# Kernel optimization log

Measured on AMD Instinct MI355X. Metric: run time of the kernel, lower is better.

## Reference

```python
import jax, jax.numpy as jnp
import numpy as np

N, E, H = 25000, 100000, 32          # nodes, edges, node/clique hidden dim
NC, A, EC = 8000, 50000, 24000       # cliques, node2clique assignments, clique edges
EEMB, CEE, L = 8, 8, 2               # edge emb dims, n layers


def segment_mean(vals, ids, num):
    s = jax.ops.segment_sum(vals, ids, num_segments=num)
    cnt = jax.ops.segment_sum(jnp.ones(ids.shape[0], vals.dtype), ids, num_segments=num)
    return s / jnp.maximum(cnt, 1.0)[:, None]


def setup_inputs() -> dict:
    key = jax.random.key(0)
    ks = jax.random.split(key, 24)
    s = 0.1  # param scale
    inp = {
        "node_features": jax.random.normal(ks[0], (N, H), jnp.float32),
        "edge_index": jax.random.randint(ks[1], (2, E), 0, N),
        "edge_features": jax.random.normal(ks[2], (E, EEMB), jnp.float32),
        "clique_features": jax.random.normal(ks[3], (NC, H), jnp.float32),
        "node2clique_index": jnp.stack([
            jax.random.randint(ks[4], (A,), 0, N),
            jax.random.randint(ks[5], (A,), 0, NC)]),
        "clique_edge_index": jax.random.randint(ks[6], (2, EC), 0, NC),
        "clique_edge_features": jax.random.normal(ks[7], (EC, CEE), jnp.float32),
        # node NNConv params (stacked over L layers)
        "nn1_w": jax.random.normal(ks[8], (L, EEMB, H)) * s,
        "nn1_b": jnp.zeros((L, H)),
        "nn2_w": jax.random.normal(ks[9], (L, H, H * H)) * s,
        "nn2_b": jnp.zeros((L, H * H)),
        "root_w": jax.random.normal(ks[10], (L, H, H)) * s,
        "root_b": jnp.zeros((L, H)),
        # Node2Clique linear
        "n2c_w": jax.random.normal(ks[11], (L, H, H)) * s,
        "n2c_b": jnp.zeros((L, H)),
        # clique NNConv params
        "cnn1_w": jax.random.normal(ks[12], (L, CEE, H)) * s,
        "cnn1_b": jnp.zeros((L, H)),
        "cnn2_w": jax.random.normal(ks[13], (L, H, H * H)) * s,
        "cnn2_b": jnp.zeros((L, H * H)),
        "croot_w": jax.random.normal(ks[14], (L, H, H)) * s,
        "croot_b": jnp.zeros((L, H)),
        # Clique2Node linear
        "c2n_w": jax.random.normal(ks[15], (L, H, H)) * s,
        "c2n_b": jnp.zeros((L, H)),
    }
    return inp


def nnconv(x, src, dst, edge_attr, w1, b1, w2, b2, rw, rb, n_out_nodes):
    # per-edge weight matrices from the edge MLP: [E, in, out]
    h = jax.nn.relu(edge_attr @ w1 + b1)
    We = (h @ w2 + b2).reshape(edge_attr.shape[0], x.shape[1], -1)
    msg = jnp.einsum('ei,eio->eo', x[src], We)           # message from source
    agg = segment_mean(msg, dst, n_out_nodes)            # mean aggregation at target
    return agg + x @ rw + rb                             # root weight + bias


def reference(node_features, edge_index, edge_features, clique_features,
              node2clique_index, clique_edge_index, clique_edge_features,
              nn1_w, nn1_b, nn2_w, nn2_b, root_w, root_b, n2c_w, n2c_b,
              cnn1_w, cnn1_b, cnn2_w, cnn2_b, croot_w, croot_b, c2n_w, c2n_b):
    x, c = node_features, clique_features
    src, dst = edge_index[0], edge_index[1]
    nid, cid = node2clique_index[0], node2clique_index[1]
    csrc, cdst = clique_edge_index[0], clique_edge_index[1]
    for l in range(L):
        # node-level edge-conditioned conv
        x = jax.nn.relu(nnconv(x, src, dst, edge_features,
                               nn1_w[l], nn1_b[l], nn2_w[l], nn2_b[l],
                               root_w[l], root_b[l], N))
        # Node2Clique: project node feats, scatter-mean into cliques
        m = x @ n2c_w[l] + n2c_b[l]
        c = c + segment_mean(m[nid], cid, NC)
        # clique-level edge-conditioned conv
        c = jax.nn.relu(nnconv(c, csrc, cdst, clique_edge_features,
                               cnn1_w[l], cnn1_b[l], cnn2_w[l], cnn2_b[l],
                               croot_w[l], croot_b[l], NC))
        # Clique2Node: project clique feats, scatter-mean back onto nodes
        m = c @ c2n_w[l] + c2n_b[l]
        x = x + segment_mean(m[cid], nid, N)
    return (x, c)
```

## Files before the change

### kernel.cpp

```cpp
#include <hip/hip_runtime.h>
#include <hip/hip_bf16.h>

typedef unsigned int u32;
typedef unsigned short u16;

#define DEVINL __device__ __forceinline__

constexpr int Nn  = 25000;
constexpr int Ee  = 100000;
constexpr int NCc = 8000;
constexpr int Aa  = 50000;
constexpr int ECc = 24000;
constexpr int TCOLS = 1088;
constexpr int WPSZ  = TCOLS*32;
constexpr int NSTR  = 580;
constexpr int NB_N = (Nn + 255)/256;
constexpr int NB_C = (NCc + 255)/256;

typedef float f32x4 __attribute__((ext_vector_type(4)));
typedef short s16x8 __attribute__((ext_vector_type(8)));

DEVINL float b2f(u16 u){ union{u32 i;float f;}v; v.i = ((u32)u)<<16; return v.f; }
DEVINL float bfl(u32 u){ union{u32 i;float f;}v; v.i = u<<16; return v.f; }
DEVINL float bfh(u32 u){ union{u32 i;float f;}v; v.i = u & 0xffff0000u; return v.f; }
DEVINL u16 f2b(float f){ union{float f;u32 i;}v; v.f=f; u32 i=v.i;
  return (u16)((i + 0x7fffu + ((i>>16)&1u)) >> 16); }
DEVINL u32 pk2(float a, float b){ return (u32)f2b(a) | ((u32)f2b(b) << 16); }
DEVINL float ldw(const void* p, long i, int f){
  return f ? ((const float*)p)[i] : b2f(((const u16*)p)[i]);
}

__global__ __launch_bounds__(256) void k_detect(const u16* __restrict__ p, int n,
                        u32* __restrict__ maxbits, int* __restrict__ zcnt,
                        int* __restrict__ done, int* __restrict__ flag){
  int i0 = blockIdx.x*256 + threadIdx.x;
  float lm = 0.f; int lz = 0;
  for (int i = i0; i < n; i += gridDim.x*256){
    u16 v = p[i];
    if (v == 0) lz++;
    lm = fmaxf(lm, fabsf(b2f(v)));
  }
  #pragma unroll
  for (int off = 32; off; off >>= 1){
    lm = fmaxf(lm, __shfl_down(lm, off));
    lz += __shfl_down(lz, off);
  }
  if ((threadIdx.x & 63) == 0){
    atomicMax(maxbits, __float_as_uint(lm));
    atomicAdd(zcnt, lz);
  }
  __syncthreads();
  if (threadIdx.x == 0){
    __threadfence();
    if (atomicAdd(done, 1) == gridDim.x - 1){
      float m = __uint_as_float(*maxbits);
      *flag = (m > 1e6f || *zcnt > n/4) ? 1 : 0;
    }
  }
}

__global__ __launch_bounds__(256) void k_conv_all(const void* __restrict__ xin, const void* __restrict__ cin,
                         float* __restrict__ xA, float* __restrict__ cA, const int* __restrict__ flag){
  int i = blockIdx.x*256 + threadIdx.x;
  int f = *flag;
  if (i < Nn*32) xA[i] = ldw(xin, i, f);
  else { i -= Nn*32; if (i < NCc*32) cA[i] = ldw(cin, i, f); }
}

__global__ __launch_bounds__(256) void k_count_all(const int* __restrict__ ei, const int* __restrict__ cei,
                          const int* __restrict__ n2c,
                          int* __restrict__ deg_nd, int* __restrict__ deg_ce,
                          int* __restrict__ deg_n2c, int* __restrict__ deg_c2n,
                          int* __restrict__ cnt_sn, int* __restrict__ cnt_sc){
  int i = blockIdx.x*256 + threadIdx.x;
  if (i < Ee)                             atomicAdd(&deg_nd[ei[Ee + i]], 1);
  else if ((i -= Ee) < ECc)               atomicAdd(&deg_ce[cei[ECc + i]], 1);
  else if ((i -= ECc) < Aa)               atomicAdd(&deg_n2c[n2c[Aa + i]], 1);
  else if ((i -= Aa) < Aa)                atomicAdd(&deg_c2n[n2c[i]], 1);
  else if ((i -= Aa) < Ee)                atomicAdd(&cnt_sn[ei[i]], 1);
  else if ((i -= Ee) < ECc)               atomicAdd(&cnt_sc[cei[i]], 1);
}

__global__ __launch_bounds__(256) void k_scan_block(
    const int* __restrict__ c0, const int* __restrict__ c1,
    const int* __restrict__ c2, const int* __restrict__ c3,
    int* __restrict__ o0, int* __restrict__ o1, int* __restrict__ o2, int* __restrict__ o3,
    int* __restrict__ b0, int* __restrict__ b1, int* __restrict__ b2, int* __restrict__ b3){
  __shared__ int s[256];
  int bid = blockIdx.x, seg, rb;
  if (bid < NB_N){ seg=0; rb=bid; }
  else if (bid < NB_N+NB_C){ seg=1; rb=bid-NB_N; }
  else if (bid < 2*NB_N+NB_C){ seg=2; rb=bid-NB_N-NB_C; }
  else { seg=3; rb=bid-2*NB_N-NB_C; }
  const int* cnt = seg==0?c0 : seg==1?c1 : seg==2?c2 : c3;
  int* offs = seg==0?o0 : seg==1?o1 : seg==2?o2 : o3;
  int* bs   = seg==0?b0 : seg==1?b1 : seg==2?b2 : b3;
  int M = (seg & 1) ? NCc : Nn;
  int tid = threadIdx.x;
  int i = rb*256 + tid;
  int v = (i < M) ? cnt[i] : 0;
  s[tid] = v; __syncthreads();
  for (int d = 1; d < 256; d <<= 1){
    int t = (tid >= d) ? s[tid-d] : 0;
    __syncthreads();
    s[tid] += t;
    __syncthreads();
  }
  if (i < M) offs[i] = s[tid] - v;
  if (tid == 255) bs[rb] = s[255];
}

__global__ __launch_bounds__(512) void k_spine(int* __restrict__ b0, int* __restrict__ b1,
                      int* __restrict__ b2, int* __restrict__ b3){
  __shared__ int s[512];
  int tid = threadIdx.x, seg = tid >> 7, lane = tid & 127;
  int NB = (seg & 1) ? NB_C : NB_N;
  int* bp = seg==0?b0 : seg==1?b1 : seg==2?b2 : b3;
  int v = (lane < NB) ? bp[lane] : 0;
  s[tid] = v; __syncthreads();
  for (int d = 1; d < 128; d <<= 1){
    int t = (lane >= d) ? s[tid-d] : 0;
    __syncthreads();
    s[tid] += t;
    __syncthreads();
  }
  if (lane < NB) bp[lane] = s[tid] - v;
}

__global__ __launch_bounds__(256) void k_scan_fix(
    int* __restrict__ o0, int* __restrict__ o1, int* __restrict__ o2, int* __restrict__ o3,
    const int* __restrict__ b0, const int* __restrict__ b1,
    const int* __restrict__ b2, const int* __restrict__ b3){
  int i = blockIdx.x*256 + threadIdx.x;
  if (i < Nn) o0[i] += b0[i >> 8];
  else if ((i -= Nn) < NCc) o1[i] += b1[i >> 8];
  else if ((i -= NCc) < Nn) o2[i] += b2[i >> 8];
  else if ((i -= Nn) < NCc) o3[i] += b3[i >> 8];
}

__global__ __launch_bounds__(256) void k_place(const int* __restrict__ ei, const int* __restrict__ cei,
                      const int* __restrict__ n2c,
                      const int* __restrict__ offs_n, const int* __restrict__ offs_c,
                      const int* __restrict__ offs_an, const int* __restrict__ offs_ac,
                      int* __restrict__ cur_n, int* __restrict__ cur_c,
                      int* __restrict__ cur_an, int* __restrict__ cur_ac,
                      int* __restrict__ perm_n, int* __restrict__ perm_c,
                      int* __restrict__ an2c, int* __restrict__ ac2n){
  int i = blockIdx.x*256 + threadIdx.x;
  if (i < Ee){
    int s = ei[i];
    perm_n[offs_n[s] + atomicAdd(&cur_n[s], 1)] = i;
  } else if ((i -= Ee) < ECc){
    int s = cei[i];
    perm_c[offs_c[s] + atomicAdd(&cur_c[s], 1)] = i;
  } else if ((i -= ECc) < Aa){
    int c = n2c[Aa + i];
    an2c[offs_ac[c] + atomicAdd(&cur_ac[c], 1)] = n2c[i];
  } else if ((i -= Aa) < Aa){
    int nd = n2c[i];
    ac2n[offs_an[nd] + atomicAdd(&cur_an[nd], 1)] = n2c[Aa + i];
  }
}

__global__ __launch_bounds__(256) void k_gather(const int* __restrict__ ei, const int* __restrict__ cei,
                       const int* __restrict__ perm_n, const int* __restrict__ perm_c,
                       const void* __restrict__ ef, const void* __restrict__ cef,
                       const int* __restrict__ flag,
                       int2* __restrict__ sdp_n, float* __restrict__ efp_n,
                       int2* __restrict__ sdp_c, float* __restrict__ efp_c){
  int i = blockIdx.x*256 + threadIdx.x;
  int f = *flag;
  if (i < Ee*8){
    int p = i >> 3, j = i & 7;
    int e = perm_n[p];
    efp_n[i] = ldw(ef, (long)e*8 + j, f);
    if (j == 0) sdp_n[p] = make_int2(ei[e], ei[Ee + e]);
  } else if ((i -= Ee*8) < ECc*8){
    int p = i >> 3, j = i & 7;
    int e = perm_c[p];
    efp_c[i] = ldw(cef, (long)e*8 + j, f);
    if (j == 0) sdp_c[p] = make_int2(cei[e], cei[ECc + e]);
  }
}

__global__ __launch_bounds__(256) void k_wpack_all(const void* __restrict__ nn2w, const void* __restrict__ nn2b,
                          const void* __restrict__ rootw,
                          const void* __restrict__ cnn2w, const void* __restrict__ cnn2b,
                          const void* __restrict__ crootw,
                          const int* __restrict__ flag, u16* __restrict__ Wp4){
  int i = blockIdx.x*256 + threadIdx.x;
  if (i >= 4*WPSZ) return;
  int set = i / WPSZ, j = i - set*WPSZ;
  int l = set >> 1, isC = set & 1;
  const void* W2 = isC ? cnn2w : nn2w;
  const void* B2 = isC ? cnn2b : nn2b;
  const void* RW = isC ? crootw : rootw;
  int f = *flag;
  int col = j >> 5, ii = j & 31;
  float v;
  if (col < 1024)      v = ldw(W2, (long)l*32768 + ((col>>5)<<10) + (ii<<5) + (col&31), f);
  else if (col < 1056) v = ldw(B2, (long)l*1024 + (ii<<5) + (col-1024), f);
  else                 v = ldw(RW, (long)l*1024 + (ii<<5) + (col-1056), f);
  Wp4[i] = f2b(v);
}

__global__ __launch_bounds__(512) void k_conv_fused(const float* __restrict__ base, int M,
                           const int2* __restrict__ sdp, const float* __restrict__ efp,
                           const int* __restrict__ offs, int E_,
                           const void* __restrict__ w1, long w1off,
                           const void* __restrict__ b1, long b1off,
                           const u16* __restrict__ Wp,
                           const void* __restrict__ rb, long rboff,
                           const int* __restrict__ flag,
                           float* __restrict__ feat_root, float* __restrict__ agg){
  __shared__ __align__(16) u32 Ts[16*NSTR];
  __shared__ float w1s[256];
  __shared__ __align__(8) u32 hws[8][4][16];
  int tid = threadIdx.x;
  int w = tid >> 6, lane = tid & 63;
  int quad = lane >> 4, lm = lane & 15;
  int n0 = blockIdx.x * 16;
  int f = *flag;
  if (tid < 256) w1s[tid] = ldw(w1, w1off + tid, f);
  float bb0 = ldw(b1, b1off + 2*lm, f);
  float bb1 = ldw(b1, b1off + 2*lm + 1, f);
  int n = n0 + lm;
  int nc = n < M ? n : M-1;
  const float* bp = base + (size_t)nc*32 + quad*8;
  s16x8 bfrag;
  #pragma unroll
  for (int j = 0; j < 8; j++) bfrag[j] = (short)f2b(bp[j]);
  #pragma unroll 1
  for (int ti = 0; ti < 9; ti++){
    int ct = w*9 + ti;
    if (ct >= 68) break;
    int colbase = ct*16;
    s16x8 afrag = *(const s16x8*)(Wp + (size_t)(colbase + lm)*32 + quad*8);
    f32x4 acc = {0.f, 0.f, 0.f, 0.f};
    acc = __builtin_amdgcn_mfma_f32_16x16x32_bf16(afrag, bfrag, acc, 0, 0, 0);
    if (ct < 66){
      int k = ct >> 1;
      int p0 = (ct & 1)*8 + quad*2;
      int idx = lm*NSTR + p0*36 + k;
      Ts[idx]      = pk2(acc[0], acc[1]);
      Ts[idx + 36] = pk2(acc[2], acc[3]);
    } else if (n < M){
      int o = (ct - 66)*16 + quad*4 - 0;
      o = (colbase + quad*4) - 1056;
      float4 v = make_float4(acc[0] + ldw(rb, rboff+o,   f),
                             acc[1] + ldw(rb, rboff+o+1, f),
                             acc[2] + ldw(rb, rboff+o+2, f),
                             acc[3] + ldw(rb, rboff+o+3, f));
      *(float4*)&feat_root[(size_t)n*32 + o] = v;
    }
  }
  __syncthreads();
  int lo = offs[n0];
  int hi = (n0 + 16 < M) ? offs[n0 + 16] : E_;
  int eg = quad, kk = lm;
  int pos = lo + w*4;
  float ef0 = 0.f, ef1 = 0.f; int sd0 = 0, sd1 = 0;
  if (lane < 32){
    int idx = pos*8 + lane;        if (idx < hi*8) ef0 = efp[idx];
    idx = (pos+32)*8 + lane;       if (idx < hi*8) ef1 = efp[idx];
  } else if (lane < 40){
    int idx = pos*2 + (lane-32);   if (idx < hi*2) sd0 = ((const int*)sdp)[idx];
    idx = (pos+32)*2 + (lane-32);  if (idx < hi*2) sd1 = ((const int*)sdp)[idx];
  }
  for (; pos < hi; pos += 32){
    int np = pos + 64;
    float ef2 = 0.f; int sd2 = 0;
    if (lane < 32){ int idx = np*8 + lane; if (idx < hi*8) ef2 = efp[idx]; }
    else if (lane < 40){ int idx = np*2 + (lane-32); if (idx < hi*2) sd2 = ((const int*)sdp)[idx]; }
    int sn = __shfl(sd0, 32 + 2*eg);
    int dn = __shfl(sd0, 33 + 2*eg);
    bool valid = (pos + eg < hi);
    int sr = sn - n0; sr = sr < 0 ? 0 : (sr > 15 ? 15 : sr);
    float a0 = bb0, a1 = bb1;
    #pragma unroll
    for (int j = 0; j < 8; j++){
      float ev = __shfl(ef0, eg*8 + j);
      a0 += ev * w1s[j*32 + 2*kk];
      a1 += ev * w1s[j*32 + 2*kk+1];
    }
    hws[w][eg][kk] = pk2(fmaxf(a0, 0.f), fmaxf(a1, 0.f));
    if (valid){
      const u32* Tr = &Ts[sr*NSTR + kk*36];
      u32 vb = Tr[32];
      float m0 = bfl(vb), m1 = bfh(vb);
      #pragma unroll
      for (int g = 0; g < 8; g++){
        uint4 tv = *(const uint4*)&Tr[g*4];
        uint2 hp = *(const uint2*)&hws[w][eg][g*2];
        float h0 = bfl(hp.x), h1 = bfh(hp.x), h2 = bfl(hp.y), h3 = bfh(hp.y);
        m0 += h0*bfl(tv.x) + h1*bfl(tv.y) + h2*bfl(tv.z) + h3*bfl(tv.w);
        m1 += h0*bfh(tv.x) + h1*bfh(tv.y) + h2*bfh(tv.z) + h3*bfh(tv.w);
      }
      float* ap = agg + (size_t)dn*32 + 2*kk;
      atomicAdd(ap,   m0);
      atomicAdd(ap+1, m1);
    }
    ef0 = ef1; sd0 = sd1; ef1 = ef2; sd1 = sd2;
  }
}

__global__ __launch_bounds__(256) void k_update_lin(const float* __restrict__ agg, const int* __restrict__ deg,
                           const float* __restrict__ feat_root, int M,
                           const void* __restrict__ w, long woff,
                           const void* __restrict__ b, long boff,
                           const int* __restrict__ flag,
                           float* __restrict__ feat, void* __restrict__ dt_out, long dt_off,
                           float* __restrict__ m_out){
  __shared__ float wsm[1024], bs[32], rows[8][33];
  int tid = threadIdx.x;
  int f = *flag;
  for (int idx = tid; idx < 1024; idx += 256) wsm[idx] = ldw(w, woff + idx, f);
  if (tid < 32) bs[tid] = ldw(b, boff + tid, f);
  int nl = tid >> 5, o = tid & 31;
  int n = blockIdx.x*8 + nl;
  long i = (long)n*32 + o;
  if (n < M){
    int dg = deg[n];
    float d = (float)(dg > 1 ? dg : 1);
    float v = fmaxf(agg[i]/d + feat_root[i], 0.f);
    rows[nl][o] = v;
    if (feat) feat[i] = v;
    if (dt_out){
      if (f) ((float*)dt_out)[dt_off + i] = v;
      else   ((u16*)dt_out)[dt_off + i]   = f2b(v);
    }
  }
  __syncthreads();
  if (n >= M) return;
  float acc = bs[o];
  #pragma unroll
  for (int j = 0; j < 32; j++) acc += rows[nl][j]*wsm[j*32+o];
  m_out[i] = acc;
}

__global__ __launch_bounds__(256) void k_segmean(const float* __restrict__ base, const float* __restrict__ m,
                        const int* __restrict__ idxarr, const int* __restrict__ offs,
                        const int* __restrict__ deg, int M, float* __restrict__ out){
  int i = blockIdx.x*256 + threadIdx.x;
  if (i >= M*32) return;
  int c = i >> 5, o = i & 31;
  int lo = offs[c], cnt = deg[c];
  float s = 0.f;
  for (int a = lo; a < lo + cnt; a++) s += m[(size_t)idxarr[a]*32 + o];
  out[i] = base[i] + s/(float)(cnt > 1 ? cnt : 1);
}

__global__ __launch_bounds__(256) void k_segmean_out(const float* __restrict__ base, const float* __restrict__ m,
                        const int* __restrict__ idxarr, const int* __restrict__ offs,
                        const int* __restrict__ deg, int M,
                        void* __restrict__ out, const int* __restrict__ flag){
  int i = blockIdx.x*256 + threadIdx.x;
  if (i >= M*32) return;
  int c = i >> 5, o = i & 31;
  int lo = offs[c], cnt = deg[c];
  float s = 0.f;
  for (int a = lo; a < lo + cnt; a++) s += m[(size_t)idxarr[a]*32 + o];
  float v = base[i] + s/(float)(cnt > 1 ? cnt : 1);
  if (*flag) ((float*)out)[i] = v;
  else       ((u16*)out)[i]   = f2b(v);
}

extern "C" void kernel_launch(void* const* d_in, const int* in_sizes, int n_in,
                              void* d_out, int out_size, void* d_ws, size_t ws_size,
                              hipStream_t stream){
  const int* ei  = (const int*)d_in[1];
  const int* n2c = (const int*)d_in[4];
  const int* cei = (const int*)d_in[5];
  const void *efr = d_in[2], *cefr = d_in[6];
  const void *nn1w = d_in[7], *nn1b = d_in[8], *nn2w = d_in[9], *nn2b = d_in[10],
             *rootw = d_in[11], *rootb = d_in[12], *n2cw = d_in[13], *n2cb = d_in[14],
             *cnn1w = d_in[15], *cnn1b = d_in[16], *cnn2w = d_in[17], *cnn2b = d_in[18],
             *crootw = d_in[19], *crootb = d_in[20], *c2nw = d_in[21], *c2nb = d_in[22];

  char* ws = (char*)d_ws;
  size_t off = 0;
  auto alloc = [&](size_t bytes){ void* p = ws + off; off += (bytes + 255) & ~(size_t)255; return p; };

  size_t zstart = off;
  float* aggE0  = (float*)alloc((size_t)Nn*32*4);
  float* aggE1  = (float*)alloc((size_t)Nn*32*4);
  float* caggE0 = (float*)alloc((size_t)NCc*32*4);
  float* caggE1 = (float*)alloc((size_t)NCc*32*4);
  int* deg_nd  = (int*)alloc((size_t)Nn*4);
  int* deg_ce  = (int*)alloc((size_t)NCc*4);
  int* deg_n2c = (int*)alloc((size_t)NCc*4);
  int* deg_c2n = (int*)alloc((size_t)Nn*4);
  int* cnt_sn  = (int*)alloc((size_t)Nn*4);
  int* cnt_sc  = (int*)alloc((size_t)NCc*4);
  int* cur_n   = (int*)alloc((size_t)Nn*4);
  int* cur_c   = (int*)alloc((size_t)NCc*4);
  int* cur_an  = (int*)alloc((size_t)Nn*4);
  int* cur_ac  = (int*)alloc((size_t)NCc*4);
  u32* maxbits = (u32*)alloc(256);
  int* zcnt = (int*)((char*)maxbits + 4);
  int* flag = (int*)((char*)maxbits + 8);
  int* done = (int*)((char*)maxbits + 12);
  size_t zbytes = off - zstart;

  float* xA  = (float*)alloc((size_t)Nn*32*4);
  float* xB  = (float*)alloc((size_t)Nn*32*4);
  float* xA1 = (float*)alloc((size_t)Nn*32*4);
  float* xC  = (float*)alloc((size_t)Nn*32*4);
  float* cA  = (float*)alloc((size_t)NCc*32*4);
  float* cB  = (float*)alloc((size_t)NCc*32*4);
  float* cC0 = (float*)alloc((size_t)NCc*32*4);
  float* cB1 = (float*)alloc((size_t)NCc*32*4);
  float* m_n = (float*)alloc((size_t)Nn*32*4);
  float* m_c = (float*)alloc((size_t)NCc*32*4);
  float* frn = (float*)alloc((size_t)Nn*32*4);
  float* frc = (float*)alloc((size_t)NCc*32*4);
  int* offs_n  = (int*)alloc((size_t)Nn*4);
  int* offs_c  = (int*)alloc((size_t)NCc*4);
  int* offs_an = (int*)alloc((size_t)Nn*4);
  int* offs_ac = (int*)alloc((size_t)NCc*4);
  int* bsum0 = (int*)alloc(512);
  int* bsum1 = (int*)alloc(512);
  int* bsum2 = (int*)alloc(512);
  int* bsum3 = (int*)alloc(512);
  int* perm_n = (int*)alloc((size_t)Ee*4);
  int* perm_c = (int*)alloc((size_t)ECc*4);
  int* an2c = (int*)alloc((size_t)Aa*4);
  int* ac2n = (int*)alloc((size_t)Aa*4);
  int2* sdp_n = (int2*)alloc((size_t)Ee*8);
  int2* sdp_c = (int2*)alloc((size_t)ECc*8);
  float* efp_n = (float*)alloc((size_t)Ee*8*4);
  float* efp_c = (float*)alloc((size_t)ECc*8*4);
  u16* Wp4 = (u16*)alloc((size_t)4*WPSZ*2);

  auto nb = [](int n){ return (n + 255)/256; };

  hipMemsetAsync(ws + zstart, 0, zbytes, stream);
  k_detect<<<256,256,0,stream>>>((const u16*)d_in[0], Nn*32, maxbits, zcnt, done, flag);
  k_conv_all<<<nb(Nn*32 + NCc*32),256,0,stream>>>(d_in[0], d_in[3], xA, cA, flag);
  k_count_all<<<nb(2*Ee + 2*ECc + 2*Aa),256,0,stream>>>(ei, cei, n2c,
      deg_nd, deg_ce, deg_n2c, deg_c2n, cnt_sn, cnt_sc);
  k_scan_block<<<2*(NB_N+NB_C),256,0,stream>>>(cnt_sn, cnt_sc, deg_c2n, deg_n2c,
      offs_n, offs_c, offs_an, offs_ac, bsum0, bsum1, bsum2, bsum3);
  k_spine<<<1,512,0,stream>>>(bsum0, bsum1, bsum2, bsum3);
  k_scan_fix<<<nb(2*(Nn+NCc)),256,0,stream>>>(offs_n, offs_c, offs_an, offs_ac,
      bsum0, bsum1, bsum2, bsum3);
  k_place<<<nb(Ee+ECc+2*Aa),256,0,stream>>>(ei, cei, n2c, offs_n, offs_c, offs_an, offs_ac,
      cur_n, cur_c, cur_an, cur_ac, perm_n, perm_c, an2c, ac2n);
  k_gather<<<nb(8*(Ee+ECc)),256,0,stream>>>(ei, cei, perm_n, perm_c, efr, cefr, flag,
      sdp_n, efp_n, sdp_c, efp_c);
  k_wpack_all<<<nb(4*WPSZ),256,0,stream>>>(nn2w, nn2b, rootw, cnn2w, cnn2b, crootw, flag, Wp4);

  int Gn = (Nn + 15)/16, Gc = (NCc + 15)/16;

  k_conv_fused<<<Gn,512,0,stream>>>(xA, Nn, sdp_n, efp_n, offs_n, Ee,
      nn1w, 0, nn1b, 0, Wp4 + 0*WPSZ, rootb, 0, flag, frn, aggE0);
  k_update_lin<<<(Nn+7)/8,256,0,stream>>>(aggE0, deg_nd, frn, Nn, n2cw, 0, n2cb, 0, flag,
      xB, nullptr, 0, m_n);
  k_segmean<<<nb(NCc*32),256,0,stream>>>(cA, m_n, an2c, offs_ac, deg_n2c, NCc, cB);
  k_conv_fused<<<Gc,512,0,stream>>>(cB, NCc, sdp_c, efp_c, offs_c, ECc,
      cnn1w, 0, cnn1b, 0, Wp4 + 1*WPSZ, crootb, 0, flag, frc, caggE0);
  k_update_lin<<<(NCc+7)/8,256,0,stream>>>(caggE0, deg_ce, frc, NCc, c2nw, 0, c2nb, 0, flag,
      cC0, nullptr, 0, m_c);
  k_segmean<<<nb(Nn*32),256,0,stream>>>(xB, m_c, ac2n, offs_an, deg_c2n, Nn, xA1);
  k_conv_fused<<<Gn,512,0,stream>>>(xA1, Nn, sdp_n, efp_n, offs_n, Ee,
      nn1w, 256, nn1b, 32, Wp4 + 2*WPSZ, rootb, 32, flag, frn, aggE1);
  k_update_lin<<<(Nn+7)/8,256,0,stream>>>(aggE1, deg_nd, frn, Nn, n2cw, 1024, n2cb, 32, flag,
      xC, nullptr, 0, m_n);
  k_segmean<<<nb(NCc*32),256,0,stream>>>(cC0, m_n, an2c, offs_ac, deg_n2c, NCc, cB1);
  k_conv_fused<<<Gc,512,0,stream>>>(cB1, NCc, sdp_c, efp_c, offs_c, ECc,
      cnn1w, 256, cnn1b, 32, Wp4 + 3*WPSZ, crootb, 32, flag, frc, caggE1);
  k_update_lin<<<(NCc+7)/8,256,0,stream>>>(caggE1, deg_ce, frc, NCc, c2nw, 1024, c2nb, 32, flag,
      nullptr, d_out, (long)Nn*32, m_c);
  k_segmean_out<<<nb(Nn*32),256,0,stream>>>(xC, m_c, ac2n, offs_an, deg_c2n, Nn, d_out, flag);
}
```

Measured before the change: 351.1 us.

## Fuse segment-mean scatters into update kernel and fold mean into conv prologue

Removes the separate segment-mean kernels: the update/linear kernel now scatters its projected rows with atomics into per-target accumulators, and the next conv kernel adds the accumulator divided by degree while loading its input. The initial input-conversion kernel is dropped, with conv reading raw inputs directly, and a final store kernel writes both outputs. The shared-memory T layout is changed to a plain bf16 row layout with a simpler single-stage prefetch. The atomic scatters add contention and nondeterministic summation order, and the new accumulator buffers must be zeroed.

```diff
diff --git a/kernel.cpp b/kernel.cpp
--- a/kernel.cpp
+++ b/kernel.cpp
@@ -13,7 +13,7 @@
 constexpr int ECc = 24000;
 constexpr int TCOLS = 1088;
 constexpr int WPSZ  = TCOLS*32;
-constexpr int NSTR  = 580;
+constexpr int TSP   = 1064;
 constexpr int NB_N = (Nn + 255)/256;
 constexpr int NB_C = (NCc + 255)/256;
 
@@ -57,14 +57,6 @@
       *flag = (m > 1e6f || *zcnt > n/4) ? 1 : 0;
     }
   }
-}
-
-__global__ __launch_bounds__(256) void k_conv_all(const void* __restrict__ xin, const void* __restrict__ cin,
-                         float* __restrict__ xA, float* __restrict__ cA, const int* __restrict__ flag){
-  int i = blockIdx.x*256 + threadIdx.x;
-  int f = *flag;
-  if (i < Nn*32) xA[i] = ldw(xin, i, f);
-  else { i -= Nn*32; if (i < NCc*32) cA[i] = ldw(cin, i, f); }
 }
 
 __global__ __launch_bounds__(256) void k_count_all(const int* __restrict__ ei, const int* __restrict__ cei,
@@ -204,7 +196,8 @@
   Wp4[i] = f2b(v);
 }
 
-__global__ __launch_bounds__(512) void k_conv_fused(const float* __restrict__ base, int M,
+__global__ __launch_bounds__(512) void k_conv_fused(const void* __restrict__ base, int braw,
+                           const float* __restrict__ addagg, const int* __restrict__ adddeg, int M,
                            const int2* __restrict__ sdp, const float* __restrict__ efp,
                            const int* __restrict__ offs, int E_,
                            const void* __restrict__ w1, long w1off,
@@ -213,7 +206,7 @@
                            const void* __restrict__ rb, long rboff,
                            const int* __restrict__ flag,
                            float* __restrict__ feat_root, float* __restrict__ agg){
-  __shared__ __align__(16) u32 Ts[16*NSTR];
+  __shared__ __align__(16) u16 Ts[16*TSP];
   __shared__ float w1s[256];
   __shared__ __align__(8) u32 hws[8][4][16];
   int tid = threadIdx.x;
@@ -221,15 +214,26 @@
   int quad = lane >> 4, lm = lane & 15;
   int n0 = blockIdx.x * 16;
   int f = *flag;
+  int bf = braw ? f : 1;
   if (tid < 256) w1s[tid] = ldw(w1, w1off + tid, f);
   float bb0 = ldw(b1, b1off + 2*lm, f);
   float bb1 = ldw(b1, b1off + 2*lm + 1, f);
   int n = n0 + lm;
   int nc = n < M ? n : M-1;
-  const float* bp = base + (size_t)nc*32 + quad*8;
+  long bidx = (long)nc*32 + quad*8;
+  float fv[8];
+  #pragma unroll
+  for (int j = 0; j < 8; j++) fv[j] = ldw(base, bidx + j, bf);
+  if (addagg){
+    int dg = adddeg[nc];
+    float d = (float)(dg > 1 ? dg : 1);
+    const float* ap = addagg + (size_t)nc*32 + quad*8;
+    #pragma unroll
+    for (int j = 0; j < 8; j++) fv[j] += ap[j]/d;
+  }
   s16x8 bfrag;
   #pragma unroll
-  for (int j = 0; j < 8; j++) bfrag[j] = (short)f2b(bp[j]);
+  for (int j = 0; j < 8; j++) bfrag[j] = (short)f2b(fv[j]);
   #pragma unroll 1
   for (int ti = 0; ti < 9; ti++){
     int ct = w*9 + ti;
@@ -238,15 +242,13 @@
     s16x8 afrag = *(const s16x8*)(Wp + (size_t)(colbase + lm)*32 + quad*8);
     f32x4 acc = {0.f, 0.f, 0.f, 0.f};
     acc = __builtin_amdgcn_mfma_f32_16x16x32_bf16(afrag, bfrag, acc, 0, 0, 0);
+    int cb = colbase + quad*4;
     if (ct < 66){
-      int k = ct >> 1;
-      int p0 = (ct & 1)*8 + quad*2;
-      int idx = lm*NSTR + p0*36 + k;
-      Ts[idx]      = pk2(acc[0], acc[1]);
-      Ts[idx + 36] = pk2(acc[2], acc[3]);
+      u32 lo = (u32)f2b(acc[0]) | ((u32)f2b(acc[1]) << 16);
+      u32 hi = (u32)f2b(acc[2]) | ((u32)f2b(acc[3]) << 16);
+      *(uint2*)&Ts[lm*TSP + cb] = make_uint2(lo, hi);
     } else if (n < M){
-      int o = (ct - 66)*16 + quad*4 - 0;
-      o = (colbase + quad*4) - 1056;
+      int o = cb - 1056;
       float4 v = make_float4(acc[0] + ldw(rb, rboff+o,   f),
                              acc[1] + ldw(rb, rboff+o+1, f),
                              acc[2] + ldw(rb, rboff+o+2, f),
@@ -259,48 +261,44 @@
   int hi = (n0 + 16 < M) ? offs[n0 + 16] : E_;
   int eg = quad, kk = lm;
   int pos = lo + w*4;
-  float ef0 = 0.f, ef1 = 0.f; int sd0 = 0, sd1 = 0;
-  if (lane < 32){
-    int idx = pos*8 + lane;        if (idx < hi*8) ef0 = efp[idx];
-    idx = (pos+32)*8 + lane;       if (idx < hi*8) ef1 = efp[idx];
-  } else if (lane < 40){
-    int idx = pos*2 + (lane-32);   if (idx < hi*2) sd0 = ((const int*)sdp)[idx];
-    idx = (pos+32)*2 + (lane-32);  if (idx < hi*2) sd1 = ((const int*)sdp)[idx];
-  }
+  float efv = 0.f; int sdv = 0;
+  if (lane < 32){ int idx = pos*8 + lane; if (idx < hi*8) efv = efp[idx]; }
+  else if (lane < 40){ int idx = pos*2 + (lane-32); if (idx < hi*2) sdv = ((const int*)sdp)[idx]; }
   for (; pos < hi; pos += 32){
-    int np = pos + 64;
-    float ef2 = 0.f; int sd2 = 0;
-    if (lane < 32){ int idx = np*8 + lane; if (idx < hi*8) ef2 = efp[idx]; }
-    else if (lane < 40){ int idx = np*2 + (lane-32); if (idx < hi*2) sd2 = ((const int*)sdp)[idx]; }
-    int sn = __shfl(sd0, 32 + 2*eg);
-    int dn = __shfl(sd0, 33 + 2*eg);
+    int np = pos + 32;
+    float efv_n = 0.f; int sdv_n = 0;
+    if (lane < 32){ int idx = np*8 + lane; if (idx < hi*8) efv_n = efp[idx]; }
+    else if (lane < 40){ int idx = np*2 + (lane-32); if (idx < hi*2) sdv_n = ((const int*)sdp)[idx]; }
+    int sn = __shfl(sdv, 32 + 2*eg);
+    int dn = __shfl(sdv, 33 + 2*eg);
     bool valid = (pos + eg < hi);
     int sr = sn - n0; sr = sr < 0 ? 0 : (sr > 15 ? 15 : sr);
     float a0 = bb0, a1 = bb1;
     #pragma unroll
     for (int j = 0; j < 8; j++){
-      float ev = __shfl(ef0, eg*8 + j);
+      float ev = __shfl(efv, eg*8 + j);
       a0 += ev * w1s[j*32 + 2*kk];
       a1 += ev * w1s[j*32 + 2*kk+1];
     }
     hws[w][eg][kk] = pk2(fmaxf(a0, 0.f), fmaxf(a1, 0.f));
     if (valid){
-      const u32* Tr = &Ts[sr*NSTR + kk*36];
-      u32 vb = Tr[32];
+      const u16* Tr = &Ts[sr*TSP];
+      u32 vb = *(const u32*)&Tr[1024 + 2*kk];
       float m0 = bfl(vb), m1 = bfh(vb);
       #pragma unroll
-      for (int g = 0; g < 8; g++){
-        uint4 tv = *(const uint4*)&Tr[g*4];
-        uint2 hp = *(const uint2*)&hws[w][eg][g*2];
-        float h0 = bfl(hp.x), h1 = bfh(hp.x), h2 = bfl(hp.y), h3 = bfh(hp.y);
-        m0 += h0*bfl(tv.x) + h1*bfl(tv.y) + h2*bfl(tv.z) + h3*bfl(tv.w);
-        m1 += h0*bfh(tv.x) + h1*bfh(tv.y) + h2*bfh(tv.z) + h3*bfh(tv.w);
+      for (int kq = 0; kq < 16; kq++){
+        u32 hp = hws[w][eg][kq];
+        float h0 = bfl(hp), h1 = bfh(hp);
+        u32 v0 = *(const u32*)&Tr[(2*kq)*32 + 2*kk];
+        u32 v1 = *(const u32*)&Tr[(2*kq+1)*32 + 2*kk];
+        m0 += h0*bfl(v0) + h1*bfl(v1);
+        m1 += h0*bfh(v0) + h1*bfh(v1);
       }
       float* ap = agg + (size_t)dn*32 + 2*kk;
       atomicAdd(ap,   m0);
       atomicAdd(ap+1, m1);
     }
-    ef0 = ef1; sd0 = sd1; ef1 = ef2; sd1 = sd2;
+    efv = efv_n; sdv = sdv_n;
   }
 }
 
@@ -309,8 +307,9 @@
                            const void* __restrict__ w, long woff,
                            const void* __restrict__ b, long boff,
                            const int* __restrict__ flag,
-                           float* __restrict__ feat, void* __restrict__ dt_out, long dt_off,
-                           float* __restrict__ m_out){
+                           float* __restrict__ feat,
+                           const int* __restrict__ sidx, const int* __restrict__ soffs,
+                           const int* __restrict__ sdeg, float* __restrict__ sagg){
   __shared__ float wsm[1024], bs[32], rows[8][33];
   int tid = threadIdx.x;
   int f = *flag;
@@ -324,43 +323,31 @@
     float d = (float)(dg > 1 ? dg : 1);
     float v = fmaxf(agg[i]/d + feat_root[i], 0.f);
     rows[nl][o] = v;
-    if (feat) feat[i] = v;
-    if (dt_out){
-      if (f) ((float*)dt_out)[dt_off + i] = v;
-      else   ((u16*)dt_out)[dt_off + i]   = f2b(v);
-    }
+    feat[i] = v;
   }
   __syncthreads();
   if (n >= M) return;
   float acc = bs[o];
   #pragma unroll
   for (int j = 0; j < 32; j++) acc += rows[nl][j]*wsm[j*32+o];
-  m_out[i] = acc;
-}
-
-__global__ __launch_bounds__(256) void k_segmean(const float* __restrict__ base, const float* __restrict__ m,
-                        const int* __restrict__ idxarr, const int* __restrict__ offs,
-                        const int* __restrict__ deg, int M, float* __restrict__ out){
-  int i = blockIdx.x*256 + threadIdx.x;
-  if (i >= M*32) return;
-  int c = i >> 5, o = i & 31;
-  int lo = offs[c], cnt = deg[c];
-  float s = 0.f;
-  for (int a = lo; a < lo + cnt; a++) s += m[(size_t)idxarr[a]*32 + o];
-  out[i] = base[i] + s/(float)(cnt > 1 ? cnt : 1);
-}
-
-__global__ __launch_bounds__(256) void k_segmean_out(const float* __restrict__ base, const float* __restrict__ m,
-                        const int* __restrict__ idxarr, const int* __restrict__ offs,
-                        const int* __restrict__ deg, int M,
-                        void* __restrict__ out, const int* __restrict__ flag){
-  int i = blockIdx.x*256 + threadIdx.x;
-  if (i >= M*32) return;
-  int c = i >> 5, o = i & 31;
-  int lo = offs[c], cnt = deg[c];
-  float s = 0.f;
-  for (int a = lo; a < lo + cnt; a++) s += m[(size_t)idxarr[a]*32 + o];
-  float v = base[i] + s/(float)(cnt > 1 ? cnt : 1);
+  int slo = soffs[n], scnt = sdeg[n];
+  for (int a = 0; a < scnt; a++)
+    atomicAdd(&sagg[(size_t)sidx[slo + a]*32 + o], acc);
+}
+
+__global__ __launch_bounds__(256) void k_store(const float* __restrict__ x, const float* __restrict__ xagg,
+                      const int* __restrict__ xdeg, const float* __restrict__ c,
+                      void* __restrict__ out, const int* __restrict__ flag){
+  int i = blockIdx.x*256 + threadIdx.x;
+  int tot = Nn*32 + NCc*32;
+  if (i >= tot) return;
+  float v;
+  if (i < Nn*32){
+    int n = i >> 5;
+    int dg = xdeg[n];
+    float d = (float)(dg > 1 ? dg : 1);
+    v = x[i] + xagg[i]/d;
+  } else v = c[i - Nn*32];
   if (*flag) ((float*)out)[i] = v;
   else       ((u16*)out)[i]   = f2b(v);
 }
@@ -386,6 +373,10 @@
   float* aggE1  = (float*)alloc((size_t)Nn*32*4);
   float* caggE0 = (float*)alloc((size_t)NCc*32*4);
   float* caggE1 = (float*)alloc((size_t)NCc*32*4);
+  float* caggS0 = (float*)alloc((size_t)NCc*32*4);
+  float* caggS1 = (float*)alloc((size_t)NCc*32*4);
+  float* aggS0  = (float*)alloc((size_t)Nn*32*4);
+  float* aggS1  = (float*)alloc((size_t)Nn*32*4);
   int* deg_nd  = (int*)alloc((size_t)Nn*4);
   int* deg_ce  = (int*)alloc((size_t)NCc*4);
   int* deg_n2c = (int*)alloc((size_t)NCc*4);
@@ -402,26 +393,18 @@
   int* done = (int*)((char*)maxbits + 12);
   size_t zbytes = off - zstart;
 
-  float* xA  = (float*)alloc((size_t)Nn*32*4);
   float* xB  = (float*)alloc((size_t)Nn*32*4);
-  float* xA1 = (float*)alloc((size_t)Nn*32*4);
   float* xC  = (float*)alloc((size_t)Nn*32*4);
-  float* cA  = (float*)alloc((size_t)NCc*32*4);
-  float* cB  = (float*)alloc((size_t)NCc*32*4);
   float* cC0 = (float*)alloc((size_t)NCc*32*4);
-  float* cB1 = (float*)alloc((size_t)NCc*32*4);
-  float* m_n = (float*)alloc((size_t)Nn*32*4);
-  float* m_c = (float*)alloc((size_t)NCc*32*4);
+  float* cC1 = (float*)alloc((size_t)NCc*32*4);
   float* frn = (float*)alloc((size_t)Nn*32*4);
   float* frc = (float*)alloc((size_t)NCc*32*4);
   int* offs_n  = (int*)alloc((size_t)Nn*4);
   int* offs_c  = (int*)alloc((size_t)NCc*4);
   int* offs_an = (int*)alloc((size_t)Nn*4);
   int* offs_ac = (int*)alloc((size_t)NCc*4);
-  int* bsum0 = (int*)alloc(512);
-  int* bsum1 = (int*)alloc(512);
-  int* bsum2 = (int*)alloc(512);
-  int* bsum3 = (int*)alloc(512);
+  int* bs0 = (int*)alloc(512); int* bs1 = (int*)alloc(512);
+  int* bs2 = (int*)alloc(512); int* bs3 = (int*)alloc(512);
   int* perm_n = (int*)alloc((size_t)Ee*4);
   int* perm_c = (int*)alloc((size_t)ECc*4);
   int* an2c = (int*)alloc((size_t)Aa*4);
@@ -436,14 +419,13 @@
 
   hipMemsetAsync(ws + zstart, 0, zbytes, stream);
   k_detect<<<256,256,0,stream>>>((const u16*)d_in[0], Nn*32, maxbits, zcnt, done, flag);
-  k_conv_all<<<nb(Nn*32 + NCc*32),256,0,stream>>>(d_in[0], d_in[3], xA, cA, flag);
   k_count_all<<<nb(2*Ee + 2*ECc + 2*Aa),256,0,stream>>>(ei, cei, n2c,
       deg_nd, deg_ce, deg_n2c, deg_c2n, cnt_sn, cnt_sc);
   k_scan_block<<<2*(NB_N+NB_C),256,0,stream>>>(cnt_sn, cnt_sc, deg_c2n, deg_n2c,
-      offs_n, offs_c, offs_an, offs_ac, bsum0, bsum1, bsum2, bsum3);
-  k_spine<<<1,512,0,stream>>>(bsum0, bsum1, bsum2, bsum3);
+      offs_n, offs_c, offs_an, offs_ac, bs0, bs1, bs2, bs3);
+  k_spine<<<1,512,0,stream>>>(bs0, bs1, bs2, bs3);
   k_scan_fix<<<nb(2*(Nn+NCc)),256,0,stream>>>(offs_n, offs_c, offs_an, offs_ac,
-      bsum0, bsum1, bsum2, bsum3);
+      bs0, bs1, bs2, bs3);
   k_place<<<nb(Ee+ECc+2*Aa),256,0,stream>>>(ei, cei, n2c, offs_n, offs_c, offs_an, offs_ac,
       cur_n, cur_c, cur_an, cur_ac, perm_n, perm_c, an2c, ac2n);
   k_gather<<<nb(8*(Ee+ECc)),256,0,stream>>>(ei, cei, perm_n, perm_c, efr, cefr, flag,
@@ -452,24 +434,21 @@
 
   int Gn = (Nn + 15)/16, Gc = (NCc + 15)/16;
 
-  k_conv_fused<<<Gn,512,0,stream>>>(xA, Nn, sdp_n, efp_n, offs_n, Ee,
+  k_conv_fused<<<Gn,512,0,stream>>>(d_in[0], 1, nullptr, nullptr, Nn, sdp_n, efp_n, offs_n, Ee,
       nn1w, 0, nn1b, 0, Wp4 + 0*WPSZ, rootb, 0, flag, frn, aggE0);
   k_update_lin<<<(Nn+7)/8,256,0,stream>>>(aggE0, deg_nd, frn, Nn, n2cw, 0, n2cb, 0, flag,
-      xB, nullptr, 0, m_n);
-  k_segmean<<<nb(NCc*32),256,0,stream>>>(cA, m_n, an2c, offs_ac, deg_n2c, NCc, cB);
-  k_conv_fused<<<Gc,512,0,stream>>>(cB, NCc, sdp_c, efp_c, offs_c, ECc,
+      xB, ac2n, offs_an, deg_c2n, caggS0);
+  k_conv_fused<<<Gc,512,0,stream>>>(d_in[3], 1, caggS0, deg_n2c, NCc, sdp_c, efp_c, offs_c, ECc,
       cnn1w, 0, cnn1b, 0, Wp4 + 1*WPSZ, crootb, 0, flag, frc, caggE0);
   k_update_lin<<<(NCc+7)/8,256,0,stream>>>(caggE0, deg_ce, frc, NCc, c2nw, 0, c2nb, 0, flag,
-      cC0, nullptr, 0, m_c);
-  k_segmean<<<nb(Nn*32),256,0,stream>>>(xB, m_c, ac2n, offs_an, deg_c2n, Nn, xA1);
-  k_conv_fused<<<Gn,512,0,stream>>>(xA1, Nn, sdp_n, efp_n, offs_n, Ee,
+      cC0, an2c, offs_ac, deg_n2c, aggS0);
+  k_conv_fused<<<Gn,512,0,stream>>>(xB, 0, aggS0, deg_c2n, Nn, sdp_n, efp_n, offs_n, Ee,
       nn1w, 256, nn1b, 32, Wp4 + 2*WPSZ, rootb, 32, flag, frn, aggE1);
   k_update_lin<<<(Nn+7)/8,256,0,stream>>>(aggE1, deg_nd, frn, Nn, n2cw, 1024, n2cb, 32, flag,
-      xC, nullptr, 0, m_n);
-  k_segmean<<<nb(NCc*32),256,0,stream>>>(cC0, m_n, an2c, offs_ac, deg_n2c, NCc, cB1);
-  k_conv_fused<<<Gc,512,0,stream>>>(cB1, NCc, sdp_c, efp_c, offs_c, ECc,
+      xC, ac2n, offs_an, deg_c2n, caggS1);
+  k_conv_fused<<<Gc,512,0,stream>>>(cC0, 0, caggS1, deg_n2c, NCc, sdp_c, efp_c, offs_c, ECc,
       cnn1w, 256, cnn1b, 32, Wp4 + 3*WPSZ, crootb, 32, flag, frc, caggE1);
   k_update_lin<<<(NCc+7)/8,256,0,stream>>>(caggE1, deg_ce, frc, NCc, c2nw, 1024, c2nb, 32, flag,
-      nullptr, d_out, (long)Nn*32, m_c);
-  k_segmean_out<<<nb(Nn*32),256,0,stream>>>(xC, m_c, ac2n, offs_an, deg_c2n, Nn, d_out, flag);
-}
+      cC1, an2c, offs_ac, deg_n2c, aggS1);
+  k_store<<<nb(Nn*32 + NCc*32),256,0,stream>>>(xC, aggS1, deg_c2n, cC1, d_out, flag);
+}
```

Measured after the change: 355.9 us. About the same (+1.4%).
